# Performance work log

Hardware: AMD Instinct MI355X
Metric: run time of the kernel (lower is better)

## Reference

```python
import jax, jax.numpy as jnp
import numpy as np
import math

T, N, P, H, E, S, R = 64, 1024, 256, 256, 512, 16, 16

def _sincos(n, d):
    pos = np.arange(n)[:, None].astype(np.float32)
    div = np.exp(np.arange(0, d, 2).astype(np.float32) * -(math.log(10000.0) / d))
    pe = np.zeros((n, d), np.float32)
    pe[:, 0::2] = np.sin(pos * div)
    pe[:, 1::2] = np.cos(pos * div)
    return jnp.asarray(pe)

def setup_inputs():
    key = jax.random.key(0)
    ks = iter(jax.random.split(key, 40))
    def w(shape, s=0.05):
        return jax.random.normal(next(ks), shape, jnp.float32) * s
    adj_seq = (jax.random.uniform(next(ks), (T, N, N)) < 0.05).astype(jnp.float32)
    return dict(
        adj_seq=adj_seq,
        pos_emb=_sincos(N, P),
        g1_Wm=w((P, H)), g1_bm=jnp.zeros((H,), jnp.float32),
        g1_Wq=w((H, H)), g1_Wk=w((H, H)), g1_gb=jnp.asarray(-1.0, jnp.float32),
        g1_Wu=w((P + H, H)), g1_bu=jnp.zeros((H,), jnp.float32),
        g1_lg=jnp.ones((H,), jnp.float32), g1_lb=jnp.zeros((H,), jnp.float32),
        g2_Wm=w((H, H)), g2_bm=jnp.zeros((H,), jnp.float32),
        g2_Wu=w((2 * H, H)), g2_bu=jnp.zeros((H,), jnp.float32),
        g2_lg=jnp.ones((H,), jnp.float32), g2_lb=jnp.zeros((H,), jnp.float32),
        m_lg=jnp.ones((H,), jnp.float32), m_lb=jnp.zeros((H,), jnp.float32),
        m_Win=w((H, 2 * E)), m_bin=jnp.zeros((2 * E,), jnp.float32),
        m_Wdelta=w((E, R)), m_bdelta=jnp.zeros((R,), jnp.float32),
        m_Wdt=w((R, E)), m_bdt=jnp.zeros((E,), jnp.float32),
        m_WB=w((E, S)), m_bB=jnp.zeros((S,), jnp.float32),
        m_WC=w((E, S)), m_bC=jnp.zeros((S,), jnp.float32),
        m_Alog=-jnp.exp(w((E, S), 0.1)),
        m_D=jnp.zeros((E,), jnp.float32),
        m_Wout=w((E, H)), m_bout=jnp.zeros((H,), jnp.float32),
    )

def _ln(x, g, b):
    mu = x.mean(-1, keepdims=True)
    v = ((x - mu) ** 2).mean(-1, keepdims=True)
    return (x - mu) / jnp.sqrt(v + 1e-5) * g + b

def reference(adj_seq, pos_emb, g1_Wm, g1_bm, g1_Wq, g1_Wk, g1_gb, g1_Wu, g1_bu,
              g1_lg, g1_lb, g2_Wm, g2_bm, g2_Wu, g2_bu, g2_lg, g2_lb,
              m_lg, m_lb, m_Win, m_bin, m_Wdelta, m_bdelta, m_Wdt, m_bdt,
              m_WB, m_bB, m_WC, m_bC, m_Alog, m_D, m_Wout, m_bout):
    scale = math.sqrt(H) * max(1.0, 1e-6)  # sqrt(d) * gate_temperature

    def encode(adj):  # adj: [N,N]
        msgs = pos_emb @ g1_Wm + g1_bm                 # [N,H]
        q = msgs @ g1_Wq
        k = msgs @ g1_Wk
        gates = jax.nn.sigmoid(q @ k.T / scale + g1_gb)
        agg = (gates * adj) @ msgs                     # gated aggregation
        x = _ln(jax.nn.relu(jnp.concatenate([pos_emb, agg], -1) @ g1_Wu + g1_bu), g1_lg, g1_lb)
        msgs2 = x @ g2_Wm + g2_bm
        agg2 = adj @ msgs2                             # ungated layer 2
        x = _ln(jax.nn.relu(jnp.concatenate([x, agg2], -1) @ g2_Wu + g2_bu), g2_lg, g2_lb)
        return x                                       # [N,H]

    seq = jax.vmap(encode)(adj_seq)                    # [T,N,H]
    x = seq.transpose(1, 0, 2)                         # [N,T,H] node-batched sequences

    # --- MambaBlock ---
    res = x
    xn = _ln(x, m_lg, m_lb)
    xp = xn @ m_Win + m_bin
    u, gate = jnp.split(xp, 2, axis=-1)                # [N,T,E] each
    u = jax.nn.silu(u)
    delta = jax.nn.softplus((u @ m_Wdelta + m_bdelta) @ m_Wdt + m_bdt)  # [N,T,E]
    Bm = u @ m_WB + m_bB                               # [N,T,S]
    Cm = u @ m_WC + m_bC                               # [N,T,S]
    A = -jnp.exp(m_Alog)                               # [E,S]

    def step(h, inp):
        u_t, d_t, B_t, C_t = inp                       # [N,E],[N,E],[N,S],[N,S]
        Ad = jnp.exp(d_t[:, :, None] * A[None])        # [N,E,S]
        h = Ad * h + d_t[:, :, None] * B_t[:, None, :] * u_t[:, :, None]
        y = jnp.einsum('ns,nes->ne', C_t, h)
        return h, y

    h0 = jnp.zeros((N, E, S), x.dtype)
    _, ys = jax.lax.scan(step, h0, (u.transpose(1, 0, 2), delta.transpose(1, 0, 2),
                                    Bm.transpose(1, 0, 2), Cm.transpose(1, 0, 2)))
    y = ys.transpose(1, 0, 2)                          # [N,T,E]
    y = (y + u * m_D) * jax.nn.silu(gate)
    out = y @ m_Wout + m_bout + res                    # [N,T,H]
    return out.transpose(1, 0, 2)                      # [T,N,H]
```

## Files before the change

### kernel.cpp

```cpp
#include <hip/hip_runtime.h>
#include <hip/hip_bf16.h>

typedef __hip_bfloat16 bf16;
typedef __attribute__((ext_vector_type(8))) short s16x8;
typedef __attribute__((ext_vector_type(4))) short s16x4;
typedef __attribute__((ext_vector_type(4))) float f32x4;

#define TT 64
#define NN_ 1024
#define EE 512

__device__ __forceinline__ float toF(float v) { return v; }
__device__ __forceinline__ float toF(bf16 v) { return __bfloat162float(v); }
__device__ __forceinline__ bf16 f2b(float v) { return __float2bfloat16(v); }

enum { EPI_F32 = 0, EPI_SIG_F32 = 1 };
enum { E_LN1 = 0, E_BF16 = 1, E_LN2 = 2, E_SILU = 3, E_OUT = 4, E_TRI = 5, E_BF16T = 6 };

template <bool TRANSB, int EPI>
__global__ __launch_bounds__(256) void gemm_k(
    const float* __restrict__ A, const float* __restrict__ B,
    float* __restrict__ outF, const float* __restrict__ bias,
    const float* __restrict__ sbeta, float alpha,
    int M, int Nn, int K, int lda, int ldb)
{
    __shared__ float As[16][68];
    __shared__ float Bs[16][68];
    const int tid = threadIdx.x;
    const int tx = tid & 15, ty = tid >> 4;
    const int m0 = blockIdx.x * 64, n0 = blockIdx.y * 64;
    float acc[4][4] = {};

    for (int k0 = 0; k0 < K; k0 += 16) {
        {
            int row = tid >> 2, kk0 = (tid & 3) * 4, grow = m0 + row;
#pragma unroll
            for (int j = 0; j < 4; j++) {
                int kk = kk0 + j, gk = k0 + kk;
                As[kk][row] = (grow < M) ? A[(size_t)grow * lda + gk] : 0.f;
            }
        }
        if (!TRANSB) {
            int kk = tid >> 4, c0 = (tid & 15) * 4;
#pragma unroll
            for (int j = 0; j < 4; j++) {
                int col = c0 + j, gn = n0 + col;
                Bs[kk][col] = (gn < Nn) ? B[(size_t)(k0 + kk) * ldb + gn] : 0.f;
            }
        } else {
            int col = tid >> 2, kk0 = (tid & 3) * 4, gn = n0 + col;
#pragma unroll
            for (int j = 0; j < 4; j++) {
                int kk = kk0 + j;
                Bs[kk][col] = (gn < Nn) ? B[(size_t)gn * ldb + (k0 + kk)] : 0.f;
            }
        }
        __syncthreads();
#pragma unroll
        for (int kk = 0; kk < 16; kk++) {
            float a[4], b[4];
#pragma unroll
            for (int i = 0; i < 4; i++) a[i] = As[kk][ty * 4 + i];
#pragma unroll
            for (int j = 0; j < 4; j++) b[j] = Bs[kk][tx * 4 + j];
#pragma unroll
            for (int i = 0; i < 4; i++)
#pragma unroll
                for (int j = 0; j < 4; j++)
                    acc[i][j] = fmaf(a[i], b[j], acc[i][j]);
        }
        __syncthreads();
    }

    float gb = (EPI == EPI_SIG_F32 && sbeta) ? sbeta[0] : 0.f;
#pragma unroll
    for (int i = 0; i < 4; i++) {
        int row = m0 + ty * 4 + i;
        if (row >= M) continue;
#pragma unroll
        for (int j = 0; j < 4; j++) {
            int col = n0 + tx * 4 + j;
            if (col >= Nn) continue;
            float v = acc[i][j];
            if (EPI == EPI_F32) {
                if (bias) v += bias[col];
                outF[(size_t)row * Nn + col] = v;
            } else {
                v = v * alpha + gb;
                outF[(size_t)row * Nn + col] = 1.f / (1.f + __expf(-v));
            }
        }
    }
}

template <int BM, int BN, bool CAT, int EPI>
__global__ __launch_bounds__(256) void mfma_k(
    const bf16* __restrict__ A1, const bf16* __restrict__ A2, unsigned rowmask,
    const bf16* __restrict__ BT, const float* __restrict__ bias,
    float* __restrict__ outF,
    bf16* __restrict__ outB, bf16* __restrict__ outB2,
    const float* __restrict__ g1, const float* __restrict__ b1,
    const float* __restrict__ g2, const float* __restrict__ b2,
    const bf16* __restrict__ resid,
    int M, int K)
{
    constexpr bool LN = (EPI == E_LN1 || EPI == E_LN2);
    constexpr int STAGE_B = (BM * 32 + BN * 32) * 2;
    constexpr int SB = LN ? (64 * 260 * 4) : STAGE_B;
    __shared__ __align__(16) char smem[SB];
    short* As = (short*)smem;
    short* Bs = As + BM * 32;
    float* Cs = (float*)smem;

    const int tid = threadIdx.x;
    const int wid = tid >> 6, lane = tid & 63;
    const int wr = (BN == 256) ? 0 : wid;
    const int wc = (BN == 256) ? wid : 0;
    const int m0 = blockIdx.x * BM, n0 = blockIdx.y * BN;
    const int srow = tid >> 2;
    const int skoff = (tid & 3) * 8;

    f32x4 acc[4][4] = {};

    for (int k0 = 0; k0 < K; k0 += 32) {
#pragma unroll
        for (int c = 0; c < BM / 64; c++) {
            int r = c * 64 + srow;
            int gr = m0 + r;
            const bf16* p;
            if (CAT) {
                int gk = k0 + skoff;
                p = (gk < 256) ? (A1 + (size_t)(gr & rowmask) * 256 + gk)
                               : (A2 + (size_t)gr * 256 + (gk - 256));
            } else {
                p = A1 + (size_t)gr * K + k0 + skoff;
            }
            *(s16x8*)&As[r * 32 + skoff] = *(const s16x8*)p;
        }
#pragma unroll
        for (int c = 0; c < BN / 64; c++) {
            int r = c * 64 + srow;
            *(s16x8*)&Bs[r * 32 + skoff] =
                *(const s16x8*)(BT + (size_t)(n0 + r) * K + k0 + skoff);
        }
        __syncthreads();
        s16x8 af[4], bf[4];
#pragma unroll
        for (int mi = 0; mi < 4; mi++)
            af[mi] = *(s16x8*)&As[(wr * 64 + mi * 16 + (lane & 15)) * 32 + (lane >> 4) * 8];
#pragma unroll
        for (int ni = 0; ni < 4; ni++)
            bf[ni] = *(s16x8*)&Bs[(wc * 64 + ni * 16 + (lane & 15)) * 32 + (lane >> 4) * 8];
#pragma unroll
        for (int mi = 0; mi < 4; mi++)
#pragma unroll
            for (int ni = 0; ni < 4; ni++)
                acc[mi][ni] = __builtin_amdgcn_mfma_f32_16x16x32_bf16(
                    af[mi], bf[ni], acc[mi][ni], 0, 0, 0);
        __syncthreads();
    }

    if (EPI == E_SILU) {
#pragma unroll
        for (int mi = 0; mi < 4; mi++)
#pragma unroll
            for (int ni = 0; ni < 4; ni++)
#pragma unroll
                for (int r = 0; r < 4; r++) {
                    int row = m0 + wr * 64 + mi * 16 + (lane >> 4) * 4 + r;
                    int col = n0 + wc * 64 + ni * 16 + (lane & 15);
                    float v = acc[mi][ni][r] + bias[col];
                    float s = v / (1.f + __expf(-v));
                    if (col < EE) outB[(size_t)row * EE + col] = f2b(s);
                    else          outB2[(size_t)row * EE + (col - EE)] = f2b(s);
                }
    } else if (EPI == E_BF16) {
#pragma unroll
        for (int mi = 0; mi < 4; mi++)
#pragma unroll
            for (int ni = 0; ni < 4; ni++)
#pragma unroll
                for (int r = 0; r < 4; r++) {
                    int row = m0 + wr * 64 + mi * 16 + (lane >> 4) * 4 + r;
                    int col = n0 + wc * 64 + ni * 16 + (lane & 15);
                    outB[(size_t)row * 256 + col] = f2b(acc[mi][ni][r] + bias[col]);
                }
    } else if (EPI == E_BF16T) {
#pragma unroll
        for (int mi = 0; mi < 4; mi++)
#pragma unroll
            for (int ni = 0; ni < 4; ni++)
#pragma unroll
                for (int r = 0; r < 4; r++) {
                    int row = m0 + wr * 64 + mi * 16 + (lane >> 4) * 4 + r;
                    int col = n0 + wc * 64 + ni * 16 + (lane & 15);
                    size_t dst = (((size_t)(row >> 10)) * 256 + col) * 1024 + (row & 1023);
                    outB[dst] = f2b(acc[mi][ni][r] + bias[col]);
                }
    } else if (EPI == E_OUT) {
#pragma unroll
        for (int mi = 0; mi < 4; mi++)
#pragma unroll
            for (int ni = 0; ni < 4; ni++)
#pragma unroll
                for (int r = 0; r < 4; r++) {
                    int row = m0 + wr * 64 + mi * 16 + (lane >> 4) * 4 + r;
                    int col = n0 + wc * 64 + ni * 16 + (lane & 15);
                    float v = acc[mi][ni][r] + bias[col] + toF(resid[(size_t)row * 256 + col]);
                    int t = row & 63, n = row >> 6;
                    outF[((size_t)t * NN_ + n) * 256 + col] = v;
                }
    } else if (EPI == E_TRI) {
#pragma unroll
        for (int mi = 0; mi < 4; mi++)
#pragma unroll
            for (int ni = 0; ni < 4; ni++)
#pragma unroll
                for (int r = 0; r < 4; r++) {
                    int row = m0 + wid * 64 + mi * 16 + (lane >> 4) * 4 + r;
                    int col = ni * 16 + (lane & 15);
                    if (col < 48) {
                        float v = acc[mi][ni][r] + bias[col];
                        outF[(size_t)row * 48 + col] = v;
                    }
                }
    } else {
#pragma unroll
        for (int mi = 0; mi < 4; mi++)
#pragma unroll
            for (int ni = 0; ni < 4; ni++)
#pragma unroll
                for (int r = 0; r < 4; r++) {
                    int rl = mi * 16 + (lane >> 4) * 4 + r;
                    int cl = wc * 64 + ni * 16 + (lane & 15);
                    Cs[rl * 260 + cl] = fmaxf(acc[mi][ni][r] + bias[cl], 0.f);
                }
        __syncthreads();
        float g1v[4], b1v[4], g2v[4], b2v[4];
#pragma unroll
        for (int i = 0; i < 4; i++) {
            g1v[i] = g1[lane * 4 + i];
            b1v[i] = b1[lane * 4 + i];
            if (EPI == E_LN2) { g2v[i] = g2[lane * 4 + i]; b2v[i] = b2[lane * 4 + i]; }
        }
        for (int rr = 0; rr < 16; rr++) {
            int rl = wid * 16 + rr;
            int grow = m0 + rl;
            float x[4];
#pragma unroll
            for (int i = 0; i < 4; i++) x[i] = Cs[rl * 260 + lane * 4 + i];
            float s = x[0] + x[1] + x[2] + x[3];
#pragma unroll
            for (int o = 1; o < 64; o <<= 1) s += __shfl_xor(s, o, 64);
            float mu = s * (1.f / 256.f);
            float d[4], ss = 0.f;
#pragma unroll
            for (int i = 0; i < 4; i++) { d[i] = x[i] - mu; ss = fmaf(d[i], d[i], ss); }
#pragma unroll
            for (int o = 1; o < 64; o <<= 1) ss += __shfl_xor(ss, o, 64);
            float inv = rsqrtf(fmaxf(ss * (1.f / 256.f), 0.f) + 1e-5f);
            float y[4];
#pragma unroll
            for (int i = 0; i < 4; i++) y[i] = d[i] * inv * g1v[i] + b1v[i];
            if (EPI == E_LN1) {
                __align__(8) bf16 pk[4];
#pragma unroll
                for (int i = 0; i < 4; i++) pk[i] = f2b(y[i]);
                *(s16x4*)&outB[(size_t)grow * 256 + lane * 4] = *(s16x4*)pk;
            } else {
                int trow = (grow & 1023) * 64 + (grow >> 10);
                __align__(8) bf16 pk[4];
#pragma unroll
                for (int i = 0; i < 4; i++) pk[i] = f2b(y[i]);
                *(s16x4*)&outB[(size_t)trow * 256 + lane * 4] = *(s16x4*)pk;
                float s2 = y[0] + y[1] + y[2] + y[3];
#pragma unroll
                for (int o = 1; o < 64; o <<= 1) s2 += __shfl_xor(s2, o, 64);
                float mu2 = s2 * (1.f / 256.f);
                float d2[4], ss2 = 0.f;
#pragma unroll
                for (int i = 0; i < 4; i++) { d2[i] = y[i] - mu2; ss2 = fmaf(d2[i], d2[i], ss2); }
#pragma unroll
                for (int o = 1; o < 64; o <<= 1) ss2 += __shfl_xor(ss2, o, 64);
                float inv2 = rsqrtf(fmaxf(ss2 * (1.f / 256.f), 0.f) + 1e-5f);
                __align__(8) bf16 pk2[4];
#pragma unroll
                for (int i = 0; i < 4; i++) pk2[i] = f2b(d2[i] * inv2 * g2v[i] + b2v[i]);
                *(s16x4*)&outB2[(size_t)trow * 256 + lane * 4] = *(s16x4*)pk2;
            }
        }
    }
}

template <bool GATED>
__global__ __launch_bounds__(256) void aggmm_k(
    const float* __restrict__ adj, const float* __restrict__ gates,
    const bf16* __restrict__ BTsrc, bf16* __restrict__ out)
{
    __shared__ __align__(16) short As[64 * 40];
    __shared__ __align__(16) short Bs[256 * 40];
    const int tid = threadIdx.x;
    const int wid = tid >> 6, lane = tid & 63;
    const int bx = blockIdx.x;
    const int srow = tid >> 2;
    const int skoff = (tid & 3) * 8;
    const size_t NN2 = (size_t)NN_ * NN_;

    size_t abase, astride;
    size_t orow0;
    const bf16* bt;
    if (GATED) {
        abase = (size_t)bx * NN_;
        astride = NN2;
        bt = BTsrc;
        orow0 = 0;
    } else {
        int t = bx >> 4, n0 = (bx & 15) * 64;
        abase = (size_t)t * NN2 + (size_t)n0 * NN_;
        astride = NN_;
        bt = BTsrc + (size_t)t * 256 * 1024;
        orow0 = (size_t)t * 1024 + n0;
    }

    f32x4 acc[4][4] = {};

    for (int k0 = 0; k0 < 1024; k0 += 32) {
        {
            const float* p = adj + abase + (size_t)srow * astride + (k0 + skoff);
            float4 v0 = *(const float4*)p;
            float4 v1 = *(const float4*)(p + 4);
            bf16* d = (bf16*)&As[srow * 40 + skoff];
            d[0] = f2b(v0.x); d[1] = f2b(v0.y); d[2] = f2b(v0.z); d[3] = f2b(v0.w);
            d[4] = f2b(v1.x); d[5] = f2b(v1.y); d[6] = f2b(v1.z); d[7] = f2b(v1.w);
        }
        if (GATED) {
            float g[8];
            const float* gp = gates + (size_t)bx * NN_ + (k0 + skoff);
#pragma unroll
            for (int i = 0; i < 8; i++) g[i] = gp[i];
#pragma unroll
            for (int c = 0; c < 4; c++) {
                int r = c * 64 + srow;
                s16x8 mv = *(const s16x8*)(bt + (size_t)r * 1024 + (k0 + skoff));
                bf16* d = (bf16*)&Bs[r * 40 + skoff];
#pragma unroll
                for (int i = 0; i < 8; i++) {
                    union { short s; bf16 b; } u;
                    u.s = mv[i];
                    d[i] = f2b(toF(u.b) * g[i]);
                }
            }
        } else {
#pragma unroll
            for (int c = 0; c < 4; c++) {
                int r = c * 64 + srow;
                *(s16x8*)&Bs[r * 40 + skoff] =
                    *(const s16x8*)(bt + (size_t)r * 1024 + (k0 + skoff));
            }
        }
        __syncthreads();
        s16x8 af[4], bf[4];
#pragma unroll
        for (int mi = 0; mi < 4; mi++)
            af[mi] = *(s16x8*)&As[(mi * 16 + (lane & 15)) * 40 + (lane >> 4) * 8];
#pragma unroll
        for (int ni = 0; ni < 4; ni++)
            bf[ni] = *(s16x8*)&Bs[(wid * 64 + ni * 16 + (lane & 15)) * 40 + (lane >> 4) * 8];
#pragma unroll
        for (int mi = 0; mi < 4; mi++)
#pragma unroll
            for (int ni = 0; ni < 4; ni++)
                acc[mi][ni] = __builtin_amdgcn_mfma_f32_16x16x32_bf16(
                    af[mi], bf[ni], acc[mi][ni], 0, 0, 0);
        __syncthreads();
    }

#pragma unroll
    for (int mi = 0; mi < 4; mi++)
#pragma unroll
        for (int ni = 0; ni < 4; ni++)
#pragma unroll
            for (int r = 0; r < 4; r++) {
                int rowl = mi * 16 + (lane >> 4) * 4 + r;
                int col = wid * 64 + ni * 16 + (lane & 15);
                size_t orow = GATED ? ((size_t)rowl * 1024 + bx) : (orow0 + rowl);
                out[orow * 256 + col] = f2b(acc[mi][ni][r]);
            }
}

__global__ __launch_bounds__(512) void scan_k(
    const bf16* __restrict__ u, const bf16* __restrict__ sg,
    const float* __restrict__ dbc,
    const float* __restrict__ Wdt, const float* __restrict__ bdt,
    const float* __restrict__ Alog, const float* __restrict__ D,
    bf16* __restrict__ yg)
{
    const int n = blockIdx.x, e = threadIdx.x;
    float a[16], wdt[16], h[16];
#pragma unroll
    for (int s = 0; s < 16; s++) {
        a[s] = -__expf(Alog[e * 16 + s]);
        h[s] = 0.f;
    }
#pragma unroll
    for (int k = 0; k < 16; k++) wdt[k] = Wdt[(size_t)k * EE + e];
    const float bdte = bdt[e], De = D[e];
    const float* __restrict__ rowp = dbc + (size_t)n * TT * 48;
    const size_t base = (size_t)n * TT * EE + e;
#pragma unroll 1
    for (int t = 0; t < TT; t++) {
        const float* __restrict__ r = rowp + t * 48;
        float acc = bdte;
#pragma unroll
        for (int k = 0; k < 16; k++) acc = fmaf(r[k], wdt[k], acc);
        float delta = (acc > 20.f) ? acc : __logf(1.f + __expf(acc));
        size_t idx = base + (size_t)t * EE;
        float uv = toF(u[idx]);
        float du = delta * uv;
        float y = 0.f;
#pragma unroll
        for (int s = 0; s < 16; s++) {
            float ad = __expf(delta * a[s]);
            h[s] = fmaf(ad, h[s], du * r[16 + s]);
            y = fmaf(r[32 + s], h[s], y);
        }
        yg[idx] = f2b((y + uv * De) * toF(sg[idx]));
    }
}

__global__ void cast_k(const float* __restrict__ in, bf16* __restrict__ out, int n) {
    int i = blockIdx.x * 256 + threadIdx.x;
    if (i < n) out[i] = f2b(in[i]);
}
__global__ void transT_k(const float* __restrict__ W, bf16* __restrict__ out, int K, int Nn) {
    int gid = blockIdx.x * 256 + threadIdx.x;
    if (gid >= K * Nn) return;
    int n = gid / K, k = gid - n * K;
    out[gid] = f2b(W[(size_t)k * Nn + n]);
}
__global__ void transmsgs_k(const float* __restrict__ msgs, bf16* __restrict__ msgsT) {
    int gid = blockIdx.x * 256 + threadIdx.x;
    int c = gid >> 10, j = gid & 1023;
    msgsT[gid] = f2b(msgs[(size_t)j * 256 + c]);
}
__global__ void wdbct_k(const float* __restrict__ Wd, const float* __restrict__ WB,
                        const float* __restrict__ WC, bf16* __restrict__ out,
                        const float* __restrict__ bd, const float* __restrict__ bB,
                        const float* __restrict__ bC, float* __restrict__ biascat) {
    int gid = blockIdx.x * 256 + threadIdx.x;
    if (gid < 48) biascat[gid] = (gid < 16) ? bd[gid] : (gid < 32) ? bB[gid - 16] : bC[gid - 32];
    if (gid >= 64 * 512) return;
    int n = gid >> 9, k = gid & 511;
    float v = 0.f;
    if (n < 16)      v = Wd[(size_t)k * 16 + n];
    else if (n < 32) v = WB[(size_t)k * 16 + (n - 16)];
    else if (n < 48) v = WC[(size_t)k * 16 + (n - 32)];
    out[gid] = f2b(v);
}

extern "C" void kernel_launch(void* const* d_in, const int* in_sizes, int n_in,
                              void* d_out, int out_size, void* d_ws, size_t ws_size,
                              hipStream_t stream)
{
    const float* adj   = (const float*)d_in[0];
    const float* pos   = (const float*)d_in[1];
    const float* g1Wm  = (const float*)d_in[2];
    const float* g1bm  = (const float*)d_in[3];
    const float* g1Wq  = (const float*)d_in[4];
    const float* g1Wk  = (const float*)d_in[5];
    const float* g1gb  = (const float*)d_in[6];
    const float* g1Wu  = (const float*)d_in[7];
    const float* g1bu  = (const float*)d_in[8];
    const float* g1lg  = (const float*)d_in[9];
    const float* g1lb  = (const float*)d_in[10];
    const float* g2Wm  = (const float*)d_in[11];
    const float* g2bm  = (const float*)d_in[12];
    const float* g2Wu  = (const float*)d_in[13];
    const float* g2bu  = (const float*)d_in[14];
    const float* g2lg  = (const float*)d_in[15];
    const float* g2lb  = (const float*)d_in[16];
    const float* mlg   = (const float*)d_in[17];
    const float* mlb   = (const float*)d_in[18];
    const float* mWin  = (const float*)d_in[19];
    const float* mbin  = (const float*)d_in[20];
    const float* mWd   = (const float*)d_in[21];
    const float* mbd   = (const float*)d_in[22];
    const float* mWdt  = (const float*)d_in[23];
    const float* mbdt  = (const float*)d_in[24];
    const float* mWB   = (const float*)d_in[25];
    const float* mbB   = (const float*)d_in[26];
    const float* mWC   = (const float*)d_in[27];
    const float* mbC   = (const float*)d_in[28];
    const float* mAlog = (const float*)d_in[29];
    const float* mD    = (const float*)d_in[30];
    const float* mWout = (const float*)d_in[31];
    const float* mbout = (const float*)d_in[32];
    float* out = (float*)d_out;
    char* ws = (char*)d_ws;

    const size_t BIGE = (size_t)TT * NN_ * 256;
    size_t o = 0;
    auto alloc = [&](size_t bytes) { size_t r = o; o += (bytes + 255) & ~(size_t)255; return r; };

    float* msgs  = (float*)(ws + alloc((size_t)NN_ * 256 * 4));
    float* q     = (float*)(ws + alloc((size_t)NN_ * 256 * 4));
    float* kk    = (float*)(ws + alloc((size_t)NN_ * 256 * 4));
    float* gates = (float*)(ws + alloc((size_t)NN_ * NN_ * 4));
    bf16*  Ra    = (bf16*)(ws + alloc(BIGE * 2));
    size_t off_x1 = alloc(BIGE * 2);
    bf16*  x1    = (bf16*)(ws + off_x1);
    bf16*  agg2  = (bf16*)(ws + alloc(BIGE * 2));
    bf16*  x2    = (bf16*)(ws + alloc(BIGE * 2));
    bf16*  yg    = (bf16*)(ws + alloc(BIGE * 2));
    bf16*  sg    = (bf16*)(ws + alloc((size_t)NN_ * TT * EE * 2));
    float* dbc   = (float*)(ws + alloc((size_t)TT * NN_ * 48 * 4));
    bf16*  u     = (bf16*)(ws + off_x1);
    bf16* posb   = (bf16*)(ws + alloc((size_t)NN_ * 256 * 2));
    bf16* g1WuT  = (bf16*)(ws + alloc((size_t)256 * 512 * 2));
    bf16* g2WmT  = (bf16*)(ws + alloc((size_t)256 * 256 * 2));
    bf16* g2WuT  = (bf16*)(ws + alloc((size_t)256 * 512 * 2));
    bf16* mWinT  = (bf16*)(ws + alloc((size_t)1024 * 256 * 2));
    bf16* mWoutT = (bf16*)(ws + alloc((size_t)256 * 512 * 2));
    bf16* WdBCT  = (bf16*)(ws + alloc((size_t)64 * 512 * 2));
    float* biascat = (float*)(ws + alloc(64 * 4));
    bf16* msgsT  = (bf16*)(ws + alloc((size_t)256 * 1024 * 2));
    bf16* msgs2T = (bf16*)(ws + alloc(BIGE * 2));

    const unsigned ALLR = 0xFFFFFFFFu;
    const int M = TT * NN_;

    cast_k<<<NN_, 256, 0, stream>>>(pos, posb, NN_ * 256);
    transT_k<<<(512 * 256 + 255) / 256, 256, 0, stream>>>(g1Wu, g1WuT, 512, 256);
    transT_k<<<(256 * 256 + 255) / 256, 256, 0, stream>>>(g2Wm, g2WmT, 256, 256);
    transT_k<<<(512 * 256 + 255) / 256, 256, 0, stream>>>(g2Wu, g2WuT, 512, 256);
    transT_k<<<(256 * 1024 + 255) / 256, 256, 0, stream>>>(mWin, mWinT, 256, 1024);
    transT_k<<<(512 * 256 + 255) / 256, 256, 0, stream>>>(mWout, mWoutT, 512, 256);
    wdbct_k<<<(64 * 512 + 255) / 256, 256, 0, stream>>>(mWd, mWB, mWC, WdBCT, mbd, mbB, mbC, biascat);

    gemm_k<false, EPI_F32><<<dim3(16, 4), 256, 0, stream>>>(
        pos, g1Wm, msgs, g1bm, nullptr, 1.f, NN_, 256, 256, 256, 256);
    transmsgs_k<<<1024, 256, 0, stream>>>(msgs, msgsT);
    gemm_k<false, EPI_F32><<<dim3(16, 4), 256, 0, stream>>>(
        msgs, g1Wq, q, nullptr, nullptr, 1.f, NN_, 256, 256, 256, 256);
    gemm_k<false, EPI_F32><<<dim3(16, 4), 256, 0, stream>>>(
        msgs, g1Wk, kk, nullptr, nullptr, 1.f, NN_, 256, 256, 256, 256);
    gemm_k<true, EPI_SIG_F32><<<dim3(16, 16), 256, 0, stream>>>(
        q, kk, gates, nullptr, g1gb, 1.f / 16.f, NN_, NN_, 256, 256, 256);
    aggmm_k<true><<<1024, 256, 0, stream>>>(adj, gates, msgsT, Ra);
    mfma_k<64, 256, true, E_LN1><<<dim3(1024, 1), 256, 0, stream>>>(
        posb, Ra, 1023u, g1WuT, g1bu, nullptr, x1, nullptr,
        g1lg, g1lb, nullptr, nullptr, nullptr, M, 512);
    mfma_k<64, 256, false, E_BF16T><<<dim3(1024, 1), 256, 0, stream>>>(
        x1, x1, ALLR, g2WmT, g2bm, nullptr, msgs2T, nullptr,
        nullptr, nullptr, nullptr, nullptr, nullptr, M, 256);
    aggmm_k<false><<<1024, 256, 0, stream>>>(adj, nullptr, msgs2T, agg2);
    mfma_k<64, 256, true, E_LN2><<<dim3(1024, 1), 256, 0, stream>>>(
        x1, agg2, ALLR, g2WuT, g2bu, nullptr, x2, Ra,
        g2lg, g2lb, mlg, mlb, nullptr, M, 512);
    mfma_k<64, 256, false, E_SILU><<<dim3(1024, 4), 256, 0, stream>>>(
        Ra, Ra, ALLR, mWinT, mbin, nullptr, u, sg,
        nullptr, nullptr, nullptr, nullptr, nullptr, M, 256);
    mfma_k<256, 64, false, E_TRI><<<dim3(256, 1), 256, 0, stream>>>(
        u, u, ALLR, WdBCT, biascat, dbc, nullptr, nullptr,
        nullptr, nullptr, nullptr, nullptr, nullptr, M, 512);
    scan_k<<<NN_, 512, 0, stream>>>(u, sg, dbc, mWdt, mbdt, mAlog, mD, yg);
    mfma_k<64, 256, false, E_OUT><<<dim3(1024, 1), 256, 0, stream>>>(
        yg, yg, ALLR, mWoutT, mbout, out, nullptr, nullptr,
        nullptr, nullptr, nullptr, nullptr, x2, M, 512);

    (void)in_sizes; (void)n_in; (void)out_size; (void)ws_size;
}
```

Before: 1.237 ms.

## Retile adjacency aggregation GEMM to 128x256 blocks with register prefetch

The aggregation kernel now computes a 128x256 output tile per block instead of 64x256, with waves laid out 2x2. The next K-slice is prefetched into registers while the current one is consumed from shared memory, and the block count is halved. For the gated pass, the gate is now applied to the adjacency tile rather than the message tile, so both passes use the same per-timestep row-block layout. The aim is better operand reuse, overlap of global loads with MFMA work, and contiguous adjacency reads. In exchange, the gate matrix is re-read once per timestep, and register and LDS use rise, as reflected in the new launch bounds.

```diff
diff --git a/kernel.cpp b/kernel.cpp
--- a/kernel.cpp
+++ b/kernel.cpp
@@ -293,98 +293,101 @@
 }
 
 template <bool GATED>
-__global__ __launch_bounds__(256) void aggmm_k(
+__global__ __launch_bounds__(256, 2) void aggmm_k(
     const float* __restrict__ adj, const float* __restrict__ gates,
     const bf16* __restrict__ BTsrc, bf16* __restrict__ out)
 {
-    __shared__ __align__(16) short As[64 * 40];
+    __shared__ __align__(16) short As[128 * 40];
     __shared__ __align__(16) short Bs[256 * 40];
     const int tid = threadIdx.x;
     const int wid = tid >> 6, lane = tid & 63;
+    const int wr = wid & 1;
+    const int wc = wid >> 1;
     const int bx = blockIdx.x;
+    const int t = bx >> 3, n0 = (bx & 7) * 128;
     const int srow = tid >> 2;
     const int skoff = (tid & 3) * 8;
     const size_t NN2 = (size_t)NN_ * NN_;
 
-    size_t abase, astride;
-    size_t orow0;
-    const bf16* bt;
-    if (GATED) {
-        abase = (size_t)bx * NN_;
-        astride = NN2;
-        bt = BTsrc;
-        orow0 = 0;
-    } else {
-        int t = bx >> 4, n0 = (bx & 15) * 64;
-        abase = (size_t)t * NN2 + (size_t)n0 * NN_;
-        astride = NN_;
-        bt = BTsrc + (size_t)t * 256 * 1024;
-        orow0 = (size_t)t * 1024 + n0;
-    }
-
-    f32x4 acc[4][4] = {};
-
+    const float* __restrict__ adjB = adj + (size_t)t * NN2 + (size_t)n0 * NN_;
+    const float* __restrict__ gB = GATED ? (gates + (size_t)n0 * NN_) : nullptr;
+    const bf16* __restrict__ bt = GATED ? BTsrc : (BTsrc + (size_t)t * 256 * 1024);
+    const size_t orow0 = (size_t)t * 1024 + n0;
+
+    f32x4 acc[4][8] = {};
+
+    float4 pa[2][2];
+    float4 pg[2][2];
+    s16x8 pb[4];
+
+    auto LOADA = [&](int k0) {
+#pragma unroll
+        for (int c = 0; c < 2; c++) {
+            const float* p = adjB + (size_t)(c * 64 + srow) * NN_ + k0 + skoff;
+            pa[c][0] = *(const float4*)p;
+            pa[c][1] = *(const float4*)(p + 4);
+            if (GATED) {
+                const float* q = gB + (size_t)(c * 64 + srow) * NN_ + k0 + skoff;
+                pg[c][0] = *(const float4*)q;
+                pg[c][1] = *(const float4*)(q + 4);
+            }
+        }
+#pragma unroll
+        for (int c = 0; c < 4; c++)
+            pb[c] = *(const s16x8*)(bt + (size_t)(c * 64 + srow) * 1024 + k0 + skoff);
+    };
+    auto STORE = [&]() {
+#pragma unroll
+        for (int c = 0; c < 2; c++) {
+            float va[8] = { pa[c][0].x, pa[c][0].y, pa[c][0].z, pa[c][0].w,
+                            pa[c][1].x, pa[c][1].y, pa[c][1].z, pa[c][1].w };
+            __align__(16) bf16 tmp[8];
+            if (GATED) {
+                float vg[8] = { pg[c][0].x, pg[c][0].y, pg[c][0].z, pg[c][0].w,
+                                pg[c][1].x, pg[c][1].y, pg[c][1].z, pg[c][1].w };
+#pragma unroll
+                for (int i = 0; i < 8; i++) tmp[i] = f2b(va[i] * vg[i]);
+            } else {
+#pragma unroll
+                for (int i = 0; i < 8; i++) tmp[i] = f2b(va[i]);
+            }
+            *(s16x8*)&As[(c * 64 + srow) * 40 + skoff] = *(s16x8*)tmp;
+        }
+#pragma unroll
+        for (int c = 0; c < 4; c++)
+            *(s16x8*)&Bs[(c * 64 + srow) * 40 + skoff] = pb[c];
+    };
+
+    LOADA(0);
+#pragma unroll 1
     for (int k0 = 0; k0 < 1024; k0 += 32) {
-        {
-            const float* p = adj + abase + (size_t)srow * astride + (k0 + skoff);
-            float4 v0 = *(const float4*)p;
-            float4 v1 = *(const float4*)(p + 4);
-            bf16* d = (bf16*)&As[srow * 40 + skoff];
-            d[0] = f2b(v0.x); d[1] = f2b(v0.y); d[2] = f2b(v0.z); d[3] = f2b(v0.w);
-            d[4] = f2b(v1.x); d[5] = f2b(v1.y); d[6] = f2b(v1.z); d[7] = f2b(v1.w);
-        }
-        if (GATED) {
-            float g[8];
-            const float* gp = gates + (size_t)bx * NN_ + (k0 + skoff);
-#pragma unroll
-            for (int i = 0; i < 8; i++) g[i] = gp[i];
-#pragma unroll
-            for (int c = 0; c < 4; c++) {
-                int r = c * 64 + srow;
-                s16x8 mv = *(const s16x8*)(bt + (size_t)r * 1024 + (k0 + skoff));
-                bf16* d = (bf16*)&Bs[r * 40 + skoff];
-#pragma unroll
-                for (int i = 0; i < 8; i++) {
-                    union { short s; bf16 b; } u;
-                    u.s = mv[i];
-                    d[i] = f2b(toF(u.b) * g[i]);
-                }
-            }
-        } else {
-#pragma unroll
-            for (int c = 0; c < 4; c++) {
-                int r = c * 64 + srow;
-                *(s16x8*)&Bs[r * 40 + skoff] =
-                    *(const s16x8*)(bt + (size_t)r * 1024 + (k0 + skoff));
-            }
-        }
-        __syncthreads();
-        s16x8 af[4], bf[4];
-#pragma unroll
-        for (int mi = 0; mi < 4; mi++)
-            af[mi] = *(s16x8*)&As[(mi * 16 + (lane & 15)) * 40 + (lane >> 4) * 8];
-#pragma unroll
-        for (int ni = 0; ni < 4; ni++)
-            bf[ni] = *(s16x8*)&Bs[(wid * 64 + ni * 16 + (lane & 15)) * 40 + (lane >> 4) * 8];
-#pragma unroll
-        for (int mi = 0; mi < 4; mi++)
-#pragma unroll
-            for (int ni = 0; ni < 4; ni++)
+        STORE();
+        __syncthreads();
+        if (k0 + 32 < 1024) LOADA(k0 + 32);
+        s16x8 af[4];
+#pragma unroll
+        for (int mi = 0; mi < 4; mi++)
+            af[mi] = *(s16x8*)&As[(wr * 64 + mi * 16 + (lane & 15)) * 40 + (lane >> 4) * 8];
+#pragma unroll
+        for (int ni = 0; ni < 8; ni++) {
+            s16x8 bfv = *(s16x8*)&Bs[(wc * 128 + ni * 16 + (lane & 15)) * 40 + (lane >> 4) * 8];
+#pragma unroll
+            for (int mi = 0; mi < 4; mi++)
                 acc[mi][ni] = __builtin_amdgcn_mfma_f32_16x16x32_bf16(
-                    af[mi], bf[ni], acc[mi][ni], 0, 0, 0);
+                    af[mi], bfv, acc[mi][ni], 0, 0, 0);
+        }
         __syncthreads();
     }
 
 #pragma unroll
     for (int mi = 0; mi < 4; mi++)
 #pragma unroll
-        for (int ni = 0; ni < 4; ni++)
+        for (int ni = 0; ni < 8; ni++)
 #pragma unroll
             for (int r = 0; r < 4; r++) {
-                int rowl = mi * 16 + (lane >> 4) * 4 + r;
-                int col = wid * 64 + ni * 16 + (lane & 15);
-                size_t orow = GATED ? ((size_t)rowl * 1024 + bx) : (orow0 + rowl);
-                out[orow * 256 + col] = f2b(acc[mi][ni][r]);
+                int rowl = wr * 64 + mi * 16 + (lane >> 4) * 4 + r;
+                int col = wc * 128 + ni * 16 + (lane & 15);
+                out[(orow0 + rowl) * 256 + col] = f2b(acc[mi][ni][r]);
             }
 }
 
@@ -546,14 +549,14 @@
         msgs, g1Wk, kk, nullptr, nullptr, 1.f, NN_, 256, 256, 256, 256);
     gemm_k<true, EPI_SIG_F32><<<dim3(16, 16), 256, 0, stream>>>(
         q, kk, gates, nullptr, g1gb, 1.f / 16.f, NN_, NN_, 256, 256, 256);
-    aggmm_k<true><<<1024, 256, 0, stream>>>(adj, gates, msgsT, Ra);
+    aggmm_k<true><<<512, 256, 0, stream>>>(adj, gates, msgsT, Ra);
     mfma_k<64, 256, true, E_LN1><<<dim3(1024, 1), 256, 0, stream>>>(
         posb, Ra, 1023u, g1WuT, g1bu, nullptr, x1, nullptr,
         g1lg, g1lb, nullptr, nullptr, nullptr, M, 512);
     mfma_k<64, 256, false, E_BF16T><<<dim3(1024, 1), 256, 0, stream>>>(
         x1, x1, ALLR, g2WmT, g2bm, nullptr, msgs2T, nullptr,
         nullptr, nullptr, nullptr, nullptr, nullptr, M, 256);
-    aggmm_k<false><<<1024, 256, 0, stream>>>(adj, nullptr, msgs2T, agg2);
+    aggmm_k<false><<<512, 256, 0, stream>>>(adj, nullptr, msgs2T, agg2);
     mfma_k<64, 256, true, E_LN2><<<dim3(1024, 1), 256, 0, stream>>>(
         x1, agg2, ALLR, g2WuT, g2bu, nullptr, x2, Ra,
         g2lg, g2lb, mlg, mlb, nullptr, M, 512);
```

Result: faster. 1.140 ms (-7.8%).
